# Performance work log

Measured on AMD Instinct MI355X. Metric: run time of the kernel, lower is better.

The kernel has to match this reference:

```python
import jax, jax.numpy as jnp
import numpy as np

EPS = 1e-5

def _weight_quant(w):
    # BitNet b1.58: per-tensor ternary quantization with STE.
    scale = 1.0 / jnp.maximum(jnp.mean(jnp.abs(w)), EPS)
    wq = jnp.clip(jnp.round(w * scale), -1.0, 1.0) / scale
    return w + jax.lax.stop_gradient(wq - w)

def _act_quant(x):
    # per-token int8 absmax quantization with STE.
    scale = 127.0 / jnp.maximum(jnp.max(jnp.abs(x), axis=-1, keepdims=True), EPS)
    xq = jnp.clip(jnp.round(x * scale), -128.0, 127.0) / scale
    return x + jax.lax.stop_gradient(xq - x)

def _bitlinear(x, w):
    # x: [..., in], w: [out, in] (torch layout)
    return jnp.einsum('bsd,hd->bsh', _act_quant(x), _weight_quant(w))

def setup_inputs() -> dict:
    key = jax.random.key(0)
    k1, k2, k3, k4 = jax.random.split(key, 4)
    B, S, D, H = 4, 2048, 2048, 5632
    x = jax.random.normal(k1, (B, S, D), dtype=jnp.float32)
    w1 = jax.random.normal(k2, (H, D), dtype=jnp.float32) * 0.02
    w2 = jax.random.normal(k3, (H, D), dtype=jnp.float32) * 0.02
    w3 = jax.random.normal(k4, (D, H), dtype=jnp.float32) * 0.02
    return {"x": x, "w1": w1, "w2": w2, "w3": w3}

def reference(x, w1, w2, w3):
    gate = jax.nn.silu(_bitlinear(x, w1))   # [B,S,H]
    up = _bitlinear(x, w2)                  # [B,S,H]
    h = gate * up                           # [B,S,H]
    return _bitlinear(h, w3)                # [B,S,D]
```

## Files before the change

### kernel.cpp

```cpp
#include <hip/hip_runtime.h>
#include <hip/hip_bf16.h>
#include <math.h>

#define EPSQ 1e-5f

typedef __attribute__((ext_vector_type(4))) int i32x4;

__device__ __forceinline__ void gload_lds16(const void* g, void* l) {
  __builtin_amdgcn_global_load_lds(
      (__attribute__((address_space(1))) void*)g,
      (__attribute__((address_space(3))) void*)l, 16, 0, 0);
}

__device__ __forceinline__ int clampi8(float v, float lo, float hi) {
  return (int)rintf(fminf(hi, fmaxf(lo, v)));
}

__global__ void wabs_kernel(const float* __restrict__ w, int n4, double* __restrict__ sum) {
  __shared__ double sm[256];
  const float4* w4 = (const float4*)w;
  double acc = 0.0;
  const int stride = gridDim.x * blockDim.x;
  for (int i = blockIdx.x * blockDim.x + threadIdx.x; i < n4; i += stride) {
    float4 v = w4[i];
    acc += (double)fabsf(v.x) + (double)fabsf(v.y) + (double)fabsf(v.z) + (double)fabsf(v.w);
  }
  sm[threadIdx.x] = acc;
  __syncthreads();
  for (int s = 128; s > 0; s >>= 1) {
    if ((int)threadIdx.x < s) sm[threadIdx.x] += sm[threadIdx.x + s];
    __syncthreads();
  }
  if (threadIdx.x == 0) atomicAdd(sum, sm[0]);
}

__global__ void wquant_kernel(const float* __restrict__ w, int n4,
                              const double* __restrict__ sum, double inv_n,
                              unsigned int* __restrict__ wq) {
  const float s = (float)fmax(*sum * inv_n, (double)EPSQ);
  const float scale = 1.0f / s;
  const int i = blockIdx.x * blockDim.x + threadIdx.x;
  if (i >= n4) return;
  float4 v = ((const float4*)w)[i];
  const int b0 = clampi8(rintf(v.x * scale), -1.f, 1.f);
  const int b1 = clampi8(rintf(v.y * scale), -1.f, 1.f);
  const int b2 = clampi8(rintf(v.z * scale), -1.f, 1.f);
  const int b3 = clampi8(rintf(v.w * scale), -1.f, 1.f);
  wq[i] = (unsigned int)((b0 & 0xff) | ((b1 & 0xff) << 8) |
                         ((b2 & 0xff) << 16) | ((b3 & 0xff) << 24));
}

__global__ void aquant_kernel(const float* __restrict__ x, int K,
                              unsigned char* __restrict__ q, float* __restrict__ arow) {
  const int row = blockIdx.x;
  const int n4 = K >> 2;
  const float4* xr = (const float4*)(x + (size_t)row * K);
  float m = 0.f;
  for (int c = threadIdx.x; c < n4; c += blockDim.x) {
    float4 v = xr[c];
    m = fmaxf(m, fmaxf(fmaxf(fabsf(v.x), fabsf(v.y)), fmaxf(fabsf(v.z), fabsf(v.w))));
  }
  __shared__ float sm[256];
  sm[threadIdx.x] = m;
  __syncthreads();
  for (int s = 128; s > 0; s >>= 1) {
    if ((int)threadIdx.x < s) sm[threadIdx.x] = fmaxf(sm[threadIdx.x], sm[threadIdx.x + s]);
    __syncthreads();
  }
  const float mv = fmaxf(sm[0], EPSQ);
  const float scale = 127.0f / mv;
  if (threadIdx.x == 0) arow[row] = mv * (1.0f / 127.0f);
  unsigned int* qr = (unsigned int*)(q + (size_t)row * K);
  for (int c = threadIdx.x; c < n4; c += blockDim.x) {
    float4 v = xr[c];
    const int b0 = clampi8(v.x * scale, -128.f, 127.f);
    const int b1 = clampi8(v.y * scale, -128.f, 127.f);
    const int b2 = clampi8(v.z * scale, -128.f, 127.f);
    const int b3 = clampi8(v.w * scale, -128.f, 127.f);
    qr[c] = (unsigned int)((b0 & 0xff) | ((b1 & 0xff) << 8) |
                           ((b2 & 0xff) << 16) | ((b3 & 0xff) << 24));
  }
}

#define BKP 64


#define PIPE_BARRIER(N)                                         \
  asm volatile("s_waitcnt vmcnt(" #N ")" ::: "memory");         \
  __builtin_amdgcn_s_barrier();                                 \
  asm volatile("" ::: "memory");

#define GU_SLOT 32768

__launch_bounds__(512, 2)
__global__ void gemm_gateup(const unsigned char* __restrict__ Aq,
                            const unsigned char* __restrict__ W1q,
                            const unsigned char* __restrict__ W2q,
                            const float* __restrict__ arow,
                            const double* __restrict__ wsum,
                            float* __restrict__ Hbuf,
                            const int N, const int K,
                            const int MBb, const int NBb) {
  __shared__ char lds[3 * GU_SLOT];

  const int tid = threadIdx.x;
  const int lane = tid & 63;
  const int wid = tid >> 6;
  const int wm = wid >> 1;
  const int wn = wid & 1;

  const int total = MBb * NBb;
  int swz = blockIdx.x;
  if ((total & 7) == 0) swz = (swz & 7) * (total >> 3) + (swz >> 3);
  const int nb = swz % NBb;
  const int mb = swz / NBb;
  const int m0 = mb * 256;
  const int n0 = nb * 128;

  const unsigned char* Ab  = Aq  + (size_t)m0 * K;
  const unsigned char* B1b = W1q + (size_t)n0 * K;
  const unsigned char* B2b = W2q + (size_t)n0 * K;

  auto stage = [&](int kt, int s) {
    const int k0 = kt * BKP;
    char* base = lds + s * GU_SLOT;
#pragma unroll
    for (int is = 0; is < 2; ++is) {
      const int p = is * 8192 + wid * 1024 + lane * 16;
      const int r = p >> 6;
      const int c = ((p >> 4) & 3) ^ ((r >> 1) & 3);
      gload_lds16(Ab + (size_t)r * K + k0 + c * 16, base + is * 8192 + wid * 1024);
    }
    {
      const int p = wid * 1024 + lane * 16;
      const int r = p >> 6;
      const int c = ((p >> 4) & 3) ^ ((r >> 1) & 3);
      const size_t go = (size_t)r * K + k0 + c * 16;
      gload_lds16(B1b + go, base + 16384 + wid * 1024);
      gload_lds16(B2b + go, base + 24576 + wid * 1024);
    }
  };

  const int c16 = lane >> 4;
  int offA[4], offB1[4], offB2[4];
#pragma unroll
  for (int i = 0; i < 4; ++i) {
    const int row = wm * 64 + i * 16 + (lane & 15);
    offA[i] = row * 64 + ((c16 ^ ((row >> 1) & 3)) << 4);
  }
#pragma unroll
  for (int j = 0; j < 4; ++j) {
    const int n = wn * 64 + j * 16 + (lane & 15);
    const int o = n * 64 + ((c16 ^ ((n >> 1) & 3)) << 4);
    offB1[j] = 16384 + o;
    offB2[j] = 24576 + o;
  }

  i32x4 acc1[4][4] = {};
  i32x4 acc2[4][4] = {};

  const int NT = K / BKP;
  stage(0, 0);
  stage(1, 1);
  PIPE_BARRIER(4)

  int s = 0, s2 = 2;
  for (int t = 0; t < NT; ++t) {
    if (t + 2 < NT) stage(t + 2, s2);
    const char* sb = lds + s * GU_SLOT;
    i32x4 af[4], b1f[4], b2f[4];
#pragma unroll
    for (int i = 0; i < 4; ++i) af[i] = *(const i32x4*)(sb + offA[i]);
#pragma unroll
    for (int j = 0; j < 4; ++j) {
      b1f[j] = *(const i32x4*)(sb + offB1[j]);
      b2f[j] = *(const i32x4*)(sb + offB2[j]);
    }
    __builtin_amdgcn_s_setprio(1);
#pragma unroll
    for (int j = 0; j < 4; ++j)
#pragma unroll
      for (int i = 0; i < 4; ++i) {
        acc1[i][j] = __builtin_amdgcn_mfma_i32_16x16x64_i8(af[i], b1f[j], acc1[i][j], 0, 0, 0);
        acc2[i][j] = __builtin_amdgcn_mfma_i32_16x16x64_i8(af[i], b2f[j], acc2[i][j], 0, 0, 0);
      }
    __builtin_amdgcn_s_setprio(0);
    if (t + 2 < NT) {
      PIPE_BARRIER(4)
    } else if (t + 1 < NT) {
      PIPE_BARRIER(0)
    }
    s = (s == 2) ? 0 : s + 1;
    s2 = (s2 == 2) ? 0 : s2 + 1;
  }

  const double inv_n = 1.0 / 11534336.0;
  const float sw1 = (float)fmax(wsum[0] * inv_n, (double)EPSQ);
  const float sw2 = (float)fmax(wsum[1] * inv_n, (double)EPSQ);
#pragma unroll
  for (int i = 0; i < 4; ++i) {
    const int rb = m0 + wm * 64 + i * 16 + (lane >> 4) * 4;
#pragma unroll
    for (int qe = 0; qe < 4; ++qe) {
      const int grow = rb + qe;
      const float a = arow[grow];
      const float f1 = a * sw1;
      const float f2 = a * sw2;
      float* hr = Hbuf + (size_t)grow * N + n0 + wn * 64 + (lane & 15);
#pragma unroll
      for (int j = 0; j < 4; ++j) {
        const float y1 = (float)acc1[i][j][qe] * f1;
        const float y2 = (float)acc2[i][j][qe] * f2;
        hr[j * 16] = (y1 / (1.0f + expf(-y1))) * y2;
      }
    }
  }
}

#define DN_SLOT 24576

__launch_bounds__(512, 2)
__global__ void gemm_down(const unsigned char* __restrict__ Aq,
                          const unsigned char* __restrict__ Wq,
                          const float* __restrict__ arow,
                          const double* __restrict__ wsum,
                          float* __restrict__ Out,
                          const int N, const int K,
                          const int MBb, const int NBb) {
  __shared__ char lds[3 * DN_SLOT];

  const int tid = threadIdx.x;
  const int lane = tid & 63;
  const int wid = tid >> 6;
  const int wm = wid >> 1;
  const int wn = wid & 1;

  const int total = MBb * NBb;
  int swz = blockIdx.x;
  if ((total & 7) == 0) swz = (swz & 7) * (total >> 3) + (swz >> 3);
  const int nb = swz % NBb;
  const int mb = swz / NBb;
  const int m0 = mb * 256;
  const int n0 = nb * 128;

  const unsigned char* Ab = Aq + (size_t)m0 * K;
  const unsigned char* Bb = Wq + (size_t)n0 * K;

  auto stage = [&](int kt, int s) {
    const int k0 = kt * BKP;
    char* base = lds + s * DN_SLOT;
#pragma unroll
    for (int is = 0; is < 2; ++is) {
      const int p = is * 8192 + wid * 1024 + lane * 16;
      const int r = p >> 6;
      const int c = ((p >> 4) & 3) ^ ((r >> 1) & 3);
      gload_lds16(Ab + (size_t)r * K + k0 + c * 16, base + is * 8192 + wid * 1024);
    }
    {
      const int p = wid * 1024 + lane * 16;
      const int r = p >> 6;
      const int c = ((p >> 4) & 3) ^ ((r >> 1) & 3);
      gload_lds16(Bb + (size_t)r * K + k0 + c * 16, base + 16384 + wid * 1024);
    }
  };

  const int c16 = lane >> 4;
  int offA[4], offB[4];
#pragma unroll
  for (int i = 0; i < 4; ++i) {
    const int row = wm * 64 + i * 16 + (lane & 15);
    offA[i] = row * 64 + ((c16 ^ ((row >> 1) & 3)) << 4);
  }
#pragma unroll
  for (int j = 0; j < 4; ++j) {
    const int n = wn * 64 + j * 16 + (lane & 15);
    offB[j] = 16384 + n * 64 + ((c16 ^ ((n >> 1) & 3)) << 4);
  }

  i32x4 acc[4][4] = {};

  const int NT = K / BKP;
  stage(0, 0);
  stage(1, 1);
  PIPE_BARRIER(3)

  int s = 0, s2 = 2;
  for (int t = 0; t < NT; ++t) {
    if (t + 2 < NT) stage(t + 2, s2);
    const char* sb = lds + s * DN_SLOT;
    i32x4 af[4], bf[4];
#pragma unroll
    for (int i = 0; i < 4; ++i) af[i] = *(const i32x4*)(sb + offA[i]);
#pragma unroll
    for (int j = 0; j < 4; ++j) bf[j] = *(const i32x4*)(sb + offB[j]);
    __builtin_amdgcn_s_setprio(1);
#pragma unroll
    for (int j = 0; j < 4; ++j)
#pragma unroll
      for (int i = 0; i < 4; ++i)
        acc[i][j] = __builtin_amdgcn_mfma_i32_16x16x64_i8(af[i], bf[j], acc[i][j], 0, 0, 0);
    __builtin_amdgcn_s_setprio(0);
    if (t + 2 < NT) {
      PIPE_BARRIER(3)
    } else if (t + 1 < NT) {
      PIPE_BARRIER(0)
    }
    s = (s == 2) ? 0 : s + 1;
    s2 = (s2 == 2) ? 0 : s2 + 1;
  }

  const double inv_n = 1.0 / 11534336.0;
  const float sw3 = (float)fmax(wsum[2] * inv_n, (double)EPSQ);
#pragma unroll
  for (int i = 0; i < 4; ++i) {
    const int rb = m0 + wm * 64 + i * 16 + (lane >> 4) * 4;
#pragma unroll
    for (int qe = 0; qe < 4; ++qe) {
      const int grow = rb + qe;
      const float f = arow[grow] * sw3;
      float* orow = Out + (size_t)grow * N + n0 + wn * 64 + (lane & 15);
#pragma unroll
      for (int j = 0; j < 4; ++j) {
        orow[j * 16] = (float)acc[i][j][qe] * f;
      }
    }
  }
}

extern "C" void kernel_launch(void* const* d_in, const int* in_sizes, int n_in,
                              void* d_out, int out_size, void* d_ws, size_t ws_size,
                              hipStream_t stream) {
  (void)n_in; (void)out_size;
  const float* x  = (const float*)d_in[0];
  const float* w1 = (const float*)d_in[1];
  const float* w2 = (const float*)d_in[2];
  const float* w3 = (const float*)d_in[3];
  float* out = (float*)d_out;

  const int D = 2048, H = 5632;
  const int M = in_sizes[0] / D;
  const long long NW = (long long)H * D;

  auto al = [](size_t v) { return (v + 255) & ~(size_t)255; };

  size_t off = 0;
  const size_t o_wsum = off; off += al(3 * sizeof(double));
  const size_t o_w1q  = off; off += al((size_t)NW);
  const size_t o_w2q  = off; off += al((size_t)NW);
  const size_t o_w3q  = off; off += al((size_t)NW);
  const size_t fixed = off;

  int Mc = 256;
  for (int cand = M; cand >= 256; cand >>= 1) {
    size_t need = fixed
                + al((size_t)cand * 4)
                + al((size_t)cand * 4)
                + al((size_t)cand * D)
                + al((size_t)cand * H * 4)
                + al((size_t)cand * H);
    if (need <= ws_size) { Mc = cand; break; }
  }

  size_t coff = fixed;
  const size_t o_arow1 = coff; coff += al((size_t)Mc * 4);
  const size_t o_arow2 = coff; coff += al((size_t)Mc * 4);
  const size_t o_qx    = coff; coff += al((size_t)Mc * D);
  const size_t o_hbuf  = coff; coff += al((size_t)Mc * H * 4);
  const size_t o_qh    = coff; coff += al((size_t)Mc * H);

  char* ws = (char*)d_ws;
  double* wsum        = (double*)(ws + o_wsum);
  unsigned char* w1q  = (unsigned char*)(ws + o_w1q);
  unsigned char* w2q  = (unsigned char*)(ws + o_w2q);
  unsigned char* w3q  = (unsigned char*)(ws + o_w3q);
  float* arow1        = (float*)(ws + o_arow1);
  float* arow2        = (float*)(ws + o_arow2);
  unsigned char* qx   = (unsigned char*)(ws + o_qx);
  float* hbuf         = (float*)(ws + o_hbuf);
  unsigned char* qh   = (unsigned char*)(ws + o_qh);

  hipMemsetAsync(wsum, 0, 3 * sizeof(double), stream);

  const int n4w = (int)(NW / 4);
  wabs_kernel<<<2048, 256, 0, stream>>>(w1, n4w, wsum + 0);
  wabs_kernel<<<2048, 256, 0, stream>>>(w2, n4w, wsum + 1);
  wabs_kernel<<<2048, 256, 0, stream>>>(w3, n4w, wsum + 2);

  const double inv_n = 1.0 / (double)NW;
  wquant_kernel<<<n4w / 256, 256, 0, stream>>>(w1, n4w, wsum + 0, inv_n, (unsigned int*)w1q);
  wquant_kernel<<<n4w / 256, 256, 0, stream>>>(w2, n4w, wsum + 1, inv_n, (unsigned int*)w2q);
  wquant_kernel<<<n4w / 256, 256, 0, stream>>>(w3, n4w, wsum + 2, inv_n, (unsigned int*)w3q);

  const int NBgu = H / 128;
  const int NBdn = D / 128;
  for (int c = 0; c < M; c += Mc) {
    const int MBb = Mc / 256;
    aquant_kernel<<<Mc, 256, 0, stream>>>(x + (size_t)c * D, D, qx, arow1);
    gemm_gateup<<<MBb * NBgu, 512, 0, stream>>>(qx, w1q, w2q, arow1, wsum,
                                                hbuf, H, D, MBb, NBgu);
    aquant_kernel<<<Mc, 256, 0, stream>>>(hbuf, H, qh, arow2);
    gemm_down<<<MBb * NBdn, 512, 0, stream>>>(qh, w3q, arow2, wsum,
                                              out + (size_t)c * D, D, H, MBb, NBdn);
  }
}
```

Baseline: 532.3 us.

## Fuse hidden row absmax into gate/up epilogue and batch weight quant kernels

The gate/up GEMM epilogue now computes a per-row abs-max of the SiLU*up output with wave shuffles and a float atomicMax into a zeroed buffer. The second activation quantization therefore no longer reads the hidden buffer twice, only once to quantize. The three weight abs-sum and three weight-quant launches are also merged into single 2D-grid launches. The cost is extra atomics and a memset per chunk. The uint atomicMax trick relies on the values being non-negative abs floats.

```diff
diff --git a/kernel.cpp b/kernel.cpp
--- a/kernel.cpp
+++ b/kernel.cpp
@@ -16,7 +16,10 @@
   return (int)rintf(fminf(hi, fmaxf(lo, v)));
 }
 
-__global__ void wabs_kernel(const float* __restrict__ w, int n4, double* __restrict__ sum) {
+__global__ void wabs3_kernel(const float* __restrict__ w1, const float* __restrict__ w2,
+                             const float* __restrict__ w3, int n4,
+                             double* __restrict__ sums) {
+  const float* w = (blockIdx.y == 0) ? w1 : (blockIdx.y == 1) ? w2 : w3;
   __shared__ double sm[256];
   const float4* w4 = (const float4*)w;
   double acc = 0.0;
@@ -31,13 +34,18 @@
     if ((int)threadIdx.x < s) sm[threadIdx.x] += sm[threadIdx.x + s];
     __syncthreads();
   }
-  if (threadIdx.x == 0) atomicAdd(sum, sm[0]);
-}
-
-__global__ void wquant_kernel(const float* __restrict__ w, int n4,
-                              const double* __restrict__ sum, double inv_n,
-                              unsigned int* __restrict__ wq) {
-  const float s = (float)fmax(*sum * inv_n, (double)EPSQ);
+  if (threadIdx.x == 0) atomicAdd(sums + blockIdx.y, sm[0]);
+}
+
+__global__ void wquant3_kernel(const float* __restrict__ w1, const float* __restrict__ w2,
+                               const float* __restrict__ w3, int n4,
+                               const double* __restrict__ sums, double inv_n,
+                               unsigned int* __restrict__ q1, unsigned int* __restrict__ q2,
+                               unsigned int* __restrict__ q3) {
+  const int wsel = blockIdx.y;
+  const float* w = (wsel == 0) ? w1 : (wsel == 1) ? w2 : w3;
+  unsigned int* wq = (wsel == 0) ? q1 : (wsel == 1) ? q2 : q3;
+  const float s = (float)fmax(sums[wsel] * inv_n, (double)EPSQ);
   const float scale = 1.0f / s;
   const int i = blockIdx.x * blockDim.x + threadIdx.x;
   if (i >= n4) return;
@@ -82,8 +90,29 @@
   }
 }
 
+__global__ void aquant_pre_kernel(const float* __restrict__ x, int K,
+                                  unsigned char* __restrict__ q, float* __restrict__ arow) {
+  const int row = blockIdx.x;
+  const float raw = arow[row];
+  __syncthreads();
+  const float mv = fmaxf(raw, EPSQ);
+  const float scale = 127.0f / mv;
+  if (threadIdx.x == 0) arow[row] = mv * (1.0f / 127.0f);
+  const int n4 = K >> 2;
+  const float4* xr = (const float4*)(x + (size_t)row * K);
+  unsigned int* qr = (unsigned int*)(q + (size_t)row * K);
+  for (int c = threadIdx.x; c < n4; c += blockDim.x) {
+    float4 v = xr[c];
+    const int b0 = clampi8(v.x * scale, -128.f, 127.f);
+    const int b1 = clampi8(v.y * scale, -128.f, 127.f);
+    const int b2 = clampi8(v.z * scale, -128.f, 127.f);
+    const int b3 = clampi8(v.w * scale, -128.f, 127.f);
+    qr[c] = (unsigned int)((b0 & 0xff) | ((b1 & 0xff) << 8) |
+                           ((b2 & 0xff) << 16) | ((b3 & 0xff) << 24));
+  }
+}
+
 #define BKP 64
-
 
 #define PIPE_BARRIER(N)                                         \
   asm volatile("s_waitcnt vmcnt(" #N ")" ::: "memory");         \
@@ -99,6 +128,7 @@
                             const float* __restrict__ arow,
                             const double* __restrict__ wsum,
                             float* __restrict__ Hbuf,
+                            float* __restrict__ hmax,
                             const int N, const int K,
                             const int MBb, const int NBb) {
   __shared__ char lds[3 * GU_SLOT];
@@ -207,12 +237,20 @@
       const float f1 = a * sw1;
       const float f2 = a * sw2;
       float* hr = Hbuf + (size_t)grow * N + n0 + wn * 64 + (lane & 15);
+      float lmax = 0.f;
 #pragma unroll
       for (int j = 0; j < 4; ++j) {
         const float y1 = (float)acc1[i][j][qe] * f1;
         const float y2 = (float)acc2[i][j][qe] * f2;
-        hr[j * 16] = (y1 / (1.0f + expf(-y1))) * y2;
+        const float h = (y1 / (1.0f + expf(-y1))) * y2;
+        hr[j * 16] = h;
+        lmax = fmaxf(lmax, fabsf(h));
       }
+#pragma unroll
+      for (int mk = 8; mk >= 1; mk >>= 1)
+        lmax = fmaxf(lmax, __shfl_xor(lmax, mk, 64));
+      if ((lane & 15) == 0)
+        atomicMax((unsigned int*)(hmax + grow), __float_as_uint(lmax));
     }
   }
 }
@@ -382,23 +420,22 @@
   hipMemsetAsync(wsum, 0, 3 * sizeof(double), stream);
 
   const int n4w = (int)(NW / 4);
-  wabs_kernel<<<2048, 256, 0, stream>>>(w1, n4w, wsum + 0);
-  wabs_kernel<<<2048, 256, 0, stream>>>(w2, n4w, wsum + 1);
-  wabs_kernel<<<2048, 256, 0, stream>>>(w3, n4w, wsum + 2);
+  wabs3_kernel<<<dim3(1024, 3), 256, 0, stream>>>(w1, w2, w3, n4w, wsum);
 
   const double inv_n = 1.0 / (double)NW;
-  wquant_kernel<<<n4w / 256, 256, 0, stream>>>(w1, n4w, wsum + 0, inv_n, (unsigned int*)w1q);
-  wquant_kernel<<<n4w / 256, 256, 0, stream>>>(w2, n4w, wsum + 1, inv_n, (unsigned int*)w2q);
-  wquant_kernel<<<n4w / 256, 256, 0, stream>>>(w3, n4w, wsum + 2, inv_n, (unsigned int*)w3q);
+  wquant3_kernel<<<dim3(n4w / 256, 3), 256, 0, stream>>>(
+      w1, w2, w3, n4w, wsum, inv_n,
+      (unsigned int*)w1q, (unsigned int*)w2q, (unsigned int*)w3q);
 
   const int NBgu = H / 128;
   const int NBdn = D / 128;
   for (int c = 0; c < M; c += Mc) {
     const int MBb = Mc / 256;
     aquant_kernel<<<Mc, 256, 0, stream>>>(x + (size_t)c * D, D, qx, arow1);
+    hipMemsetAsync(arow2, 0, (size_t)Mc * 4, stream);
     gemm_gateup<<<MBb * NBgu, 512, 0, stream>>>(qx, w1q, w2q, arow1, wsum,
-                                                hbuf, H, D, MBb, NBgu);
-    aquant_kernel<<<Mc, 256, 0, stream>>>(hbuf, H, qh, arow2);
+                                                hbuf, arow2, H, D, MBb, NBgu);
+    aquant_pre_kernel<<<Mc, 256, 0, stream>>>(hbuf, H, qh, arow2);
     gemm_down<<<MBb * NBdn, 512, 0, stream>>>(qh, w3q, arow2, wsum,
                                               out + (size_t)c * D, D, H, MBb, NBdn);
   }
```

New measurement: 492.8 us. 1.08x faster.
